# Performance work log

Hardware: AMD Instinct MI355X
Metric: run time of the kernel (lower is better)

The kernel has to match this reference:

```python
import jax, jax.numpy as jnp
import numpy as np
import math

H, D = 8, 16
O = H * D  # out_channels = 128
N_TYPES = 2
EDGE_META = [(0, 1), (1, 0)]  # (src_type, dst_type) per edge type: user->item, item->user

def _segment_softmax(alpha, dst, n):
    # PyG softmax over incoming edges grouped by destination node
    amax = jax.ops.segment_max(alpha, dst, num_segments=n)
    amax = jnp.where(jnp.isfinite(amax), amax, 0.0)
    ex = jnp.exp(alpha - amax[dst])
    den = jax.ops.segment_sum(ex, dst, num_segments=n)
    return ex / (den[dst] + 1e-16)

def setup_inputs():
    key = jax.random.key(0)
    ks = jax.random.split(key, 8)
    N, E, I = 50000, 500000, 128
    s = 1.0 / math.sqrt(I)
    sd = 1.0 / math.sqrt(D)
    return {
        "x": jax.random.normal(ks[0], (N_TYPES, N, I), jnp.float32),
        "k_w": jax.random.normal(ks[1], (N_TYPES, O, I), jnp.float32) * s,
        "k_b": jnp.zeros((N_TYPES, O), jnp.float32),
        "q_w": jax.random.normal(ks[2], (N_TYPES, O, I), jnp.float32) * s,
        "q_b": jnp.zeros((N_TYPES, O), jnp.float32),
        "v_w": jax.random.normal(ks[3], (N_TYPES, O, I), jnp.float32) * s,
        "v_b": jnp.zeros((N_TYPES, O), jnp.float32),
        "a_w": jax.random.normal(ks[4], (N_TYPES, O, O), jnp.float32) * s,
        "a_b": jnp.zeros((N_TYPES, O), jnp.float32),
        "skip": jnp.ones((N_TYPES,), jnp.float32),
        "a_rel": jax.random.normal(ks[5], (2, H, D, D), jnp.float32) * sd,
        "m_rel": jax.random.normal(ks[6], (2, H, D, D), jnp.float32) * sd,
        "p_rel": jnp.ones((2, H), jnp.float32),
        "ln_g": jnp.ones((O,), jnp.float32),
        "ln_b": jnp.zeros((O,), jnp.float32),
        "edge_index": jax.random.randint(ks[7], (2, 2, E), 0, N, jnp.int32),
    }

def reference(x, k_w, k_b, q_w, q_b, v_w, v_b, a_w, a_b, skip, a_rel, m_rel, p_rel, ln_g, ln_b, edge_index):
    N = x.shape[1]
    lin = lambda xi, w, b: xi @ w.T + b
    # per-node-type K/Q/V projections -> [T, N, H, D]
    k = jnp.stack([lin(x[t], k_w[t], k_b[t]) for t in range(N_TYPES)]).reshape(N_TYPES, N, H, D)
    q = jnp.stack([lin(x[t], q_w[t], q_b[t]) for t in range(N_TYPES)]).reshape(N_TYPES, N, H, D)
    v = jnp.stack([lin(x[t], v_w[t], v_b[t]) for t in range(N_TYPES)]).reshape(N_TYPES, N, H, D)
    agg = jnp.zeros((N_TYPES, N, O), x.dtype)
    for e, (st, dt) in enumerate(EDGE_META):
        src, dst = edge_index[e, 0], edge_index[e, 1]
        ke = jnp.einsum('nhd,hde->nhe', k[st], a_rel[e])  # relation-transformed keys
        ve = jnp.einsum('nhd,hde->nhe', v[st], m_rel[e])  # relation-transformed values
        alpha = jnp.einsum('ehd,ehd->eh', q[dt][dst], ke[src]) * p_rel[e] / math.sqrt(D)
        alpha = _segment_softmax(alpha, dst, N)  # [E, H]
        msg = (ve[src] * alpha[..., None]).reshape(-1, O)
        agg = agg.at[dt].add(jax.ops.segment_sum(msg, dst, num_segments=N))
    outs = []
    for t in range(N_TYPES):
        o = lin(jax.nn.gelu(agg[t], approximate=False), a_w[t], a_b[t])
        beta = jax.nn.sigmoid(skip[t])
        o = beta * o + (1.0 - beta) * x[t]  # HGT skip (out_channels == in_channels)
        o = jax.nn.relu(o)
        mu = jnp.mean(o, axis=-1, keepdims=True)
        var = jnp.mean((o - mu) ** 2, axis=-1, keepdims=True)
        o = (o - mu) / jnp.sqrt(var + 1e-5) * ln_g + ln_b  # LayerNorm; dropout = identity (eval)
        outs.append(o)
    return jnp.stack(outs)  # [2, N, 128]
```

## Files before the change

kernel.cpp:

```cpp
#include <hip/hip_runtime.h>
#include <math.h>


#define EB_STRIDE 40

typedef __attribute__((ext_vector_type(8))) short short8;
typedef __attribute__((ext_vector_type(4))) float floatx4;

union S8U { uint4 u; short8 s; };

__device__ __forceinline__ float bf2f(unsigned int bits16) {
  union { unsigned int i; float f; } u; u.i = bits16 << 16; return u.f;
}
__device__ __forceinline__ float bf2f_hi(unsigned int u) {
  union { unsigned int i; float f; } v; v.i = u & 0xffff0000u; return v.f;
}
__device__ __forceinline__ unsigned int f2bf(float f) {
  union { float ff; unsigned int i; } u; u.ff = f;
  unsigned int x = u.i;
  x += 0x7fffu + ((x >> 16) & 1u);
  return x >> 16;
}

__global__ void fuse_weights(
    const float* __restrict__ k_w, const float* __restrict__ k_b,
    const float* __restrict__ q_w, const float* __restrict__ q_b,
    const float* __restrict__ v_w, const float* __restrict__ v_b,
    const float* __restrict__ a_w, const float* __restrict__ a_b,
    const float* __restrict__ a_rel, const float* __restrict__ m_rel,
    const float* __restrict__ p_rel,
    unsigned short* __restrict__ Wfb, float* __restrict__ Bf,
    int* __restrict__ cnt, int nC)
{
  int tid = blockIdx.x * 256 + threadIdx.x;
  if (tid < nC) cnt[tid] = 0;
  if (tid >= 2 * 4 * 128 * 128) return;
  int t   = tid >> 16;
  int rem = tid & 65535;
  int m   = rem >> 14;
  int o   = (rem >> 7) & 127;
  int i   = rem & 127;
  float w, bias;
  if (m == 0) {
    w    = q_w[t * 16384 + o * 128 + i];
    bias = q_b[t * 128 + o];
  } else if (m == 3) {
    w    = a_w[t * 16384 + o * 128 + i];
    bias = a_b[t * 128 + o];
  } else {
    const float* bw  = (m == 1) ? k_w : v_w;
    const float* bb  = (m == 1) ? k_b : v_b;
    const float* rel = (m == 1) ? a_rel : m_rel;
    int h = o >> 4, eo = o & 15;
    float s = 0.f, sb = 0.f;
    #pragma unroll
    for (int d = 0; d < 16; ++d) {
      float r = rel[t * 2048 + h * 256 + d * 16 + eo];
      s  += bw[t * 16384 + (h * 16 + d) * 128 + i] * r;
      sb += bb[t * 128 + h * 16 + d] * r;
    }
    if (m == 1) {
      float sc = p_rel[t * 8 + h] * 0.25f;
      s *= sc; sb *= sc;
    }
    w = s; bias = sb;
  }
  Wfb[tid] = (unsigned short)f2bf(w);
  if (i == 0) Bf[t * 512 + m * 128 + o] = bias;
}

__global__ __launch_bounds__(256) void qkv_fill(
    const float* __restrict__ x, const unsigned short* __restrict__ Wfb,
    const float* __restrict__ Bf, unsigned short* __restrict__ qbuf,
    unsigned short* __restrict__ kvbuf,
    const int* __restrict__ ei, int* __restrict__ cnt, int* __restrict__ ebuf,
    int Nn, int E, int Gg)
{
  const int b = blockIdx.x;
  const int tid = threadIdx.x;

  if (b >= Gg) {
    int f = b - Gg;
    int e = f & 1;
    int i = (f >> 1) * 256 + tid;
    if (i < E) {
      int src = ei[(size_t)e * 2 * E + i];
      int dst = ei[(size_t)e * 2 * E + E + i];
      int bk = (1 - e) * Nn + dst;
      int pos = atomicAdd(&cnt[bk], 1);
      if (pos < EB_STRIDE) ebuf[(size_t)bk * EB_STRIDE + pos] = src;
    }
    return;
  }

  const int t = b & 1;
  const int m0 = (b >> 1) * 64;
  const int lane = tid & 63, w = tid >> 6;
  const int col = lane & 15, quad = lane >> 4;

  int rA = m0 + w * 16 + col;
  if (rA >= Nn) rA = Nn - 1;
  const float* arow = x + ((size_t)t * Nn + rA) * 128;

  const unsigned short* Wq = Wfb + (((size_t)(t * 4 + 0)) << 14);
  const unsigned short* Wk = Wfb + (((size_t)(t * 4 + 1)) << 14);
  const unsigned short* Wv = Wfb + (((size_t)(t * 4 + 2)) << 14);

  floatx4 aq[8], ak[8], av[8];
  #pragma unroll
  for (int ni = 0; ni < 8; ++ni) {
    aq[ni] = (floatx4)(0.f); ak[ni] = (floatx4)(0.f); av[ni] = (floatx4)(0.f);
  }

  #pragma unroll
  for (int k0 = 0; k0 < 128; k0 += 32) {
    int ko = k0 + quad * 8;
    float4 f0 = *(const float4*)(arow + ko);
    float4 f1 = *(const float4*)(arow + ko + 4);
    S8U a;
    a.u.x = f2bf(f0.x) | (f2bf(f0.y) << 16);
    a.u.y = f2bf(f0.z) | (f2bf(f0.w) << 16);
    a.u.z = f2bf(f1.x) | (f2bf(f1.y) << 16);
    a.u.w = f2bf(f1.z) | (f2bf(f1.w) << 16);
    #pragma unroll
    for (int ni = 0; ni < 8; ++ni) {
      size_t boff = (size_t)(ni * 16 + col) * 128 + ko;
      short8 bq = *(const short8*)(Wq + boff);
      short8 bk = *(const short8*)(Wk + boff);
      short8 bv = *(const short8*)(Wv + boff);
      aq[ni] = __builtin_amdgcn_mfma_f32_16x16x32_bf16(a.s, bq, aq[ni], 0, 0, 0);
      ak[ni] = __builtin_amdgcn_mfma_f32_16x16x32_bf16(a.s, bk, ak[ni], 0, 0, 0);
      av[ni] = __builtin_amdgcn_mfma_f32_16x16x32_bf16(a.s, bv, av[ni], 0, 0, 0);
    }
  }

  float bq_n[8], bk_n[8], bv_n[8];
  #pragma unroll
  for (int ni = 0; ni < 8; ++ni) {
    bq_n[ni] = Bf[t * 512 + 0 * 128 + ni * 16 + col];
    bk_n[ni] = Bf[t * 512 + 1 * 128 + ni * 16 + col];
    bv_n[ni] = Bf[t * 512 + 2 * 128 + ni * 16 + col];
  }

  unsigned int* kvp = (unsigned int*)kvbuf + ((size_t)t * Nn) * 128;
  #pragma unroll
  for (int reg = 0; reg < 4; ++reg) {
    int row = m0 + w * 16 + quad * 4 + reg;
    if (row >= Nn) continue;
    unsigned short* qp = qbuf + ((size_t)t * Nn + row) * 128 + col;
    unsigned int* cp = kvp + (size_t)row * 128 + col;
    #pragma unroll
    for (int ni = 0; ni < 8; ++ni) {
      qp[ni * 16] = (unsigned short)f2bf(aq[ni][reg] + bq_n[ni]);
      unsigned int kbits = f2bf(ak[ni][reg] + bk_n[ni]);
      unsigned int vbits = f2bf(av[ni][reg] + bv_n[ni]);
      cp[ni * 16] = (vbits << 16) | kbits;
    }
  }
}

__global__ __launch_bounds__(256) void gather_fused(
    const unsigned short* __restrict__ qbuf, const unsigned short* __restrict__ kvbuf,
    const int* __restrict__ cnt, const int* __restrict__ ebuf,
    unsigned short* __restrict__ gbuf, int N)
{
  int wid = (blockIdx.x * 256 + threadIdx.x) >> 6;
  int l = threadIdx.x & 63;
  if (wid >= 2 * N) return;
  int dt = (wid >= N) ? 1 : 0;
  int e  = 1 - dt;
  int deg = cnt[wid]; if (deg > EB_STRIDE) deg = EB_STRIDE;
  int g = l >> 4, gl = l & 15;

  uint4 qr = *(const uint4*)(qbuf + (size_t)wid * 128 + 8 * gl);
  float qv[8];
  qv[0] = bf2f(qr.x & 0xffffu); qv[1] = bf2f(qr.x >> 16);
  qv[2] = bf2f(qr.y & 0xffffu); qv[3] = bf2f(qr.y >> 16);
  qv[4] = bf2f(qr.z & 0xffffu); qv[5] = bf2f(qr.z >> 16);
  qv[6] = bf2f(qr.w & 0xffffu); qv[7] = bf2f(qr.w >> 16);

  const unsigned short* kvbase = kvbuf + ((size_t)e * N) * 256;
  const int* eb = ebuf + (size_t)wid * EB_STRIDE;
  int mysrc = (l < deg) ? eb[l] : 0;

  float acc[8];
  #pragma unroll
  for (int c = 0; c < 8; ++c) acc[c] = 0.f;
  float den = 0.f;

  for (int j0 = 0; j0 < deg; j0 += 4) {
    int j = j0 + g;
    bool valid = j < deg;
    int src = __shfl(mysrc, valid ? j : 0, 64);
    const unsigned short* kv = kvbase + (size_t)src * 256 + 16 * gl;
    uint4 a = *(const uint4*)kv;
    uint4 b = *(const uint4*)(kv + 8);
    float p;
    p = qv[0] * bf2f(a.x & 0xffffu);
    p = fmaf(qv[1], bf2f(a.y & 0xffffu), p);
    p = fmaf(qv[2], bf2f(a.z & 0xffffu), p);
    p = fmaf(qv[3], bf2f(a.w & 0xffffu), p);
    p = fmaf(qv[4], bf2f(b.x & 0xffffu), p);
    p = fmaf(qv[5], bf2f(b.y & 0xffffu), p);
    p = fmaf(qv[6], bf2f(b.z & 0xffffu), p);
    p = fmaf(qv[7], bf2f(b.w & 0xffffu), p);
    float pt = p + __shfl_xor(p, 1, 64);
    float ex = valid ? __expf(pt) : 0.f;
    den += ex;
    acc[0] = fmaf(ex, bf2f_hi(a.x), acc[0]);
    acc[1] = fmaf(ex, bf2f_hi(a.y), acc[1]);
    acc[2] = fmaf(ex, bf2f_hi(a.z), acc[2]);
    acc[3] = fmaf(ex, bf2f_hi(a.w), acc[3]);
    acc[4] = fmaf(ex, bf2f_hi(b.x), acc[4]);
    acc[5] = fmaf(ex, bf2f_hi(b.y), acc[5]);
    acc[6] = fmaf(ex, bf2f_hi(b.z), acc[6]);
    acc[7] = fmaf(ex, bf2f_hi(b.w), acc[7]);
  }

  #pragma unroll
  for (int off = 16; off < 64; off <<= 1) {
    #pragma unroll
    for (int c = 0; c < 8; ++c) acc[c] += __shfl_xor(acc[c], off, 64);
    den += __shfl_xor(den, off, 64);
  }

  if (g == 0) {
    float rden = 1.f / (den + 1e-16f);
    unsigned short r[8];
    #pragma unroll
    for (int c = 0; c < 8; ++c) {
      float gg = acc[c] * rden;
      r[c] = (unsigned short)f2bf(0.5f * gg * (1.f + erff(gg * 0.70710678118654752f)));
    }
    unsigned short* op = gbuf + (size_t)wid * 128 + 8 * gl;
    *(ushort4*)op       = make_ushort4(r[0], r[1], r[2], r[3]);
    *(ushort4*)(op + 4) = make_ushort4(r[4], r[5], r[6], r[7]);
  }
}

__global__ __launch_bounds__(256) void gemm_ln(
    const unsigned short* __restrict__ gbuf, const unsigned short* __restrict__ Wfb,
    const float* __restrict__ Bf, const float* __restrict__ x,
    const float* __restrict__ skip, const float* __restrict__ ln_g,
    const float* __restrict__ ln_b, float* __restrict__ outp, int Nn)
{
  const int tid = threadIdx.x;
  const int t = blockIdx.x & 1;
  const int m0 = (blockIdx.x >> 1) * 64;
  const int lane = tid & 63, w = tid >> 6;
  const int col = lane & 15, quad = lane >> 4;

  int rA = m0 + w * 16 + col;
  if (rA >= Nn) rA = Nn - 1;
  const unsigned short* arow = gbuf + ((size_t)t * Nn + rA) * 128;
  const unsigned short* Bm = Wfb + (((size_t)(t * 4 + 3)) << 14);

  floatx4 acc[8];
  #pragma unroll
  for (int ni = 0; ni < 8; ++ni) acc[ni] = (floatx4)(0.f);

  #pragma unroll
  for (int k0 = 0; k0 < 128; k0 += 32) {
    int ko = k0 + quad * 8;
    short8 a = *(const short8*)(arow + ko);
    #pragma unroll
    for (int ni = 0; ni < 8; ++ni) {
      short8 bb = *(const short8*)(Bm + (size_t)(ni * 16 + col) * 128 + ko);
      acc[ni] = __builtin_amdgcn_mfma_f32_16x16x32_bf16(a, bb, acc[ni], 0, 0, 0);
    }
  }

  const float* Bv = Bf + t * 512 + 3 * 128;
  float bias_n[8], g_n[8], b_n[8];
  #pragma unroll
  for (int ni = 0; ni < 8; ++ni) {
    bias_n[ni] = Bv[ni * 16 + col];
    g_n[ni]    = ln_g[ni * 16 + col];
    b_n[ni]    = ln_b[ni * 16 + col];
  }
  float sv = skip[t];
  float beta = 1.f / (1.f + __expf(-sv));
  const float* xt = x + (size_t)t * Nn * 128;
  float* op = outp + (size_t)t * Nn * 128;

  #pragma unroll
  for (int reg = 0; reg < 4; ++reg) {
    int row = m0 + w * 16 + quad * 4 + reg;
    if (row >= Nn) continue;
    const float* xr = xt + (size_t)row * 128;
    float vals[8], s = 0.f;
    #pragma unroll
    for (int ni = 0; ni < 8; ++ni) {
      float o = acc[ni][reg] + bias_n[ni];
      float v = fmaxf(beta * o + (1.f - beta) * xr[ni * 16 + col], 0.f);
      vals[ni] = v; s += v;
    }
    #pragma unroll
    for (int off = 1; off < 16; off <<= 1) s += __shfl_xor(s, off, 64);
    float mu = s * 0.0078125f;
    float sq = 0.f;
    #pragma unroll
    for (int ni = 0; ni < 8; ++ni) { float d = vals[ni] - mu; sq += d * d; }
    #pragma unroll
    for (int off = 1; off < 16; off <<= 1) sq += __shfl_xor(sq, off, 64);
    float rstd = rsqrtf(sq * 0.0078125f + 1e-5f);
    float* orow = op + (size_t)row * 128 + col;
    #pragma unroll
    for (int ni = 0; ni < 8; ++ni)
      orow[ni * 16] = (vals[ni] - mu) * rstd * g_n[ni] + b_n[ni];
  }
}

extern "C" void kernel_launch(void* const* d_in, const int* in_sizes, int n_in,
                              void* d_out, int out_size, void* d_ws, size_t ws_size,
                              hipStream_t stream) {
  const float* x     = (const float*)d_in[0];
  const float* k_w   = (const float*)d_in[1];
  const float* k_b   = (const float*)d_in[2];
  const float* q_w   = (const float*)d_in[3];
  const float* q_b   = (const float*)d_in[4];
  const float* v_w   = (const float*)d_in[5];
  const float* v_b   = (const float*)d_in[6];
  const float* a_w   = (const float*)d_in[7];
  const float* a_b   = (const float*)d_in[8];
  const float* skip  = (const float*)d_in[9];
  const float* a_rel = (const float*)d_in[10];
  const float* m_rel = (const float*)d_in[11];
  const float* p_rel = (const float*)d_in[12];
  const float* ln_g  = (const float*)d_in[13];
  const float* ln_b  = (const float*)d_in[14];
  const int* ei      = (const int*)d_in[15];
  float* out         = (float*)d_out;

  const int N = in_sizes[0] / 256;
  const int E = in_sizes[15] / 4;

  unsigned short* Wfb = (unsigned short*)d_ws;
  float* Bf = (float*)(Wfb + 2 * 4 * 128 * 128);
  unsigned short* qbuf = (unsigned short*)(Bf + 2 * 4 * 128);
  unsigned short* kvbuf = qbuf + (size_t)2 * N * 128;
  int* cnt  = (int*)(kvbuf + (size_t)2 * N * 256);
  int* ebuf = cnt + (size_t)2 * N;
  unsigned short* gbuf = (unsigned short*)(ebuf + (size_t)2 * N * EB_STRIDE);

  fuse_weights<<<(2 * 4 * 128 * 128 + 255) / 256, 256, 0, stream>>>(
      k_w, k_b, q_w, q_b, v_w, v_b, a_w, a_b, a_rel, m_rel, p_rel, Wfb, Bf,
      cnt, 2 * N);

  int Mb = (N + 63) / 64;
  int Gg = Mb * 2;
  int Fb = 2 * ((E + 255) / 256);
  qkv_fill<<<Gg + Fb, 256, 0, stream>>>(
      x, Wfb, Bf, qbuf, kvbuf, ei, cnt, ebuf, N, E, Gg);

  gather_fused<<<(2 * N * 64 + 255) / 256, 256, 0, stream>>>(
      qbuf, kvbuf, cnt, ebuf, gbuf, N);

  gemm_ln<<<Gg, 256, 0, stream>>>(
      gbuf, Wfb, Bf, x, skip, ln_g, ln_b, out, N);
}
```

Before: 350.5 us.

## Stage weight matrices in LDS and process Q/K/V projections sequentially

Result: faster. 313.9 us (-10.4%).

```diff
diff --git a/kernel.cpp b/kernel.cpp
--- a/kernel.cpp
+++ b/kernel.cpp
@@ -76,6 +76,7 @@
     const int* __restrict__ ei, int* __restrict__ cnt, int* __restrict__ ebuf,
     int Nn, int E, int Gg)
 {
+  __shared__ alignas(16) unsigned short Bls[128][136];
   const int b = blockIdx.x;
   const int tid = threadIdx.x;
 
@@ -97,24 +98,15 @@
   const int m0 = (b >> 1) * 64;
   const int lane = tid & 63, w = tid >> 6;
   const int col = lane & 15, quad = lane >> 4;
+  const int morder[3] = {1, 2, 0};
 
   int rA = m0 + w * 16 + col;
   if (rA >= Nn) rA = Nn - 1;
   const float* arow = x + ((size_t)t * Nn + rA) * 128;
-
-  const unsigned short* Wq = Wfb + (((size_t)(t * 4 + 0)) << 14);
-  const unsigned short* Wk = Wfb + (((size_t)(t * 4 + 1)) << 14);
-  const unsigned short* Wv = Wfb + (((size_t)(t * 4 + 2)) << 14);
-
-  floatx4 aq[8], ak[8], av[8];
-  #pragma unroll
-  for (int ni = 0; ni < 8; ++ni) {
-    aq[ni] = (floatx4)(0.f); ak[ni] = (floatx4)(0.f); av[ni] = (floatx4)(0.f);
-  }
-
-  #pragma unroll
-  for (int k0 = 0; k0 < 128; k0 += 32) {
-    int ko = k0 + quad * 8;
+  short8 afrag[4];
+  #pragma unroll
+  for (int kk = 0; kk < 4; ++kk) {
+    int ko = kk * 32 + quad * 8;
     float4 f0 = *(const float4*)(arow + ko);
     float4 f1 = *(const float4*)(arow + ko + 4);
     S8U a;
@@ -122,39 +114,72 @@
     a.u.y = f2bf(f0.z) | (f2bf(f0.w) << 16);
     a.u.z = f2bf(f1.x) | (f2bf(f1.y) << 16);
     a.u.w = f2bf(f1.z) | (f2bf(f1.w) << 16);
-    #pragma unroll
-    for (int ni = 0; ni < 8; ++ni) {
-      size_t boff = (size_t)(ni * 16 + col) * 128 + ko;
-      short8 bq = *(const short8*)(Wq + boff);
-      short8 bk = *(const short8*)(Wk + boff);
-      short8 bv = *(const short8*)(Wv + boff);
-      aq[ni] = __builtin_amdgcn_mfma_f32_16x16x32_bf16(a.s, bq, aq[ni], 0, 0, 0);
-      ak[ni] = __builtin_amdgcn_mfma_f32_16x16x32_bf16(a.s, bk, ak[ni], 0, 0, 0);
-      av[ni] = __builtin_amdgcn_mfma_f32_16x16x32_bf16(a.s, bv, av[ni], 0, 0, 0);
-    }
-  }
-
-  float bq_n[8], bk_n[8], bv_n[8];
-  #pragma unroll
-  for (int ni = 0; ni < 8; ++ni) {
-    bq_n[ni] = Bf[t * 512 + 0 * 128 + ni * 16 + col];
-    bk_n[ni] = Bf[t * 512 + 1 * 128 + ni * 16 + col];
-    bv_n[ni] = Bf[t * 512 + 2 * 128 + ni * 16 + col];
-  }
-
-  unsigned int* kvp = (unsigned int*)kvbuf + ((size_t)t * Nn) * 128;
-  #pragma unroll
-  for (int reg = 0; reg < 4; ++reg) {
-    int row = m0 + w * 16 + quad * 4 + reg;
-    if (row >= Nn) continue;
-    unsigned short* qp = qbuf + ((size_t)t * Nn + row) * 128 + col;
-    unsigned int* cp = kvp + (size_t)row * 128 + col;
-    #pragma unroll
-    for (int ni = 0; ni < 8; ++ni) {
-      qp[ni * 16] = (unsigned short)f2bf(aq[ni][reg] + bq_n[ni]);
-      unsigned int kbits = f2bf(ak[ni][reg] + bk_n[ni]);
-      unsigned int vbits = f2bf(av[ni][reg] + bv_n[ni]);
-      cp[ni * 16] = (vbits << 16) | kbits;
+    afrag[kk] = a.s;
+  }
+
+  unsigned int kpack[8][2];
+  float bias_n[8];
+
+  for (int mi_ = 0; mi_ < 3; ++mi_) {
+    int m = morder[mi_];
+    __syncthreads();
+    {
+      int r = tid & 127, h = tid >> 7;
+      const unsigned short* wp = Wfb + (((size_t)(t * 4 + m)) << 14) + r * 128 + h * 64;
+      #pragma unroll
+      for (int j = 0; j < 8; ++j)
+        *(uint4*)&Bls[r][h * 64 + j * 8] = ((const uint4*)wp)[j];
+    }
+    __syncthreads();
+
+    floatx4 acc[8];
+    #pragma unroll
+    for (int ni = 0; ni < 8; ++ni) acc[ni] = (floatx4)(0.f);
+
+    #pragma unroll
+    for (int kk = 0; kk < 4; ++kk) {
+      int ko = kk * 32 + quad * 8;
+      #pragma unroll
+      for (int ni = 0; ni < 8; ++ni) {
+        short8 bb = *(const short8*)&Bls[ni * 16 + col][ko];
+        acc[ni] = __builtin_amdgcn_mfma_f32_16x16x32_bf16(afrag[kk], bb, acc[ni], 0, 0, 0);
+      }
+    }
+
+    const float* Bv = Bf + t * 512 + m * 128;
+    #pragma unroll
+    for (int ni = 0; ni < 8; ++ni) bias_n[ni] = Bv[ni * 16 + col];
+
+    if (m == 1) {
+      #pragma unroll
+      for (int ni = 0; ni < 8; ++ni) {
+        kpack[ni][0] = f2bf(acc[ni][0] + bias_n[ni]) | (f2bf(acc[ni][1] + bias_n[ni]) << 16);
+        kpack[ni][1] = f2bf(acc[ni][2] + bias_n[ni]) | (f2bf(acc[ni][3] + bias_n[ni]) << 16);
+      }
+    } else if (m == 2) {
+      unsigned int* kvp = (unsigned int*)kvbuf + ((size_t)t * Nn) * 128;
+      #pragma unroll
+      for (int reg = 0; reg < 4; ++reg) {
+        int row = m0 + w * 16 + quad * 4 + reg;
+        if (row >= Nn) continue;
+        unsigned int* cp = kvp + (size_t)row * 128 + col;
+        #pragma unroll
+        for (int ni = 0; ni < 8; ++ni) {
+          unsigned int kbits = (kpack[ni][reg >> 1] >> ((reg & 1) * 16)) & 0xffffu;
+          unsigned int vbits = f2bf(acc[ni][reg] + bias_n[ni]);
+          cp[ni * 16] = (vbits << 16) | kbits;
+        }
+      }
+    } else {
+      #pragma unroll
+      for (int reg = 0; reg < 4; ++reg) {
+        int row = m0 + w * 16 + quad * 4 + reg;
+        if (row >= Nn) continue;
+        unsigned short* cp = qbuf + ((size_t)t * Nn + row) * 128 + col;
+        #pragma unroll
+        for (int ni = 0; ni < 8; ++ni)
+          cp[ni * 16] = (unsigned short)f2bf(acc[ni][reg] + bias_n[ni]);
+      }
     }
   }
 }
@@ -244,6 +269,7 @@
     const float* __restrict__ skip, const float* __restrict__ ln_g,
     const float* __restrict__ ln_b, float* __restrict__ outp, int Nn)
 {
+  __shared__ alignas(16) unsigned short Bls[128][136];
   const int tid = threadIdx.x;
   const int t = blockIdx.x & 1;
   const int m0 = (blockIdx.x >> 1) * 64;
@@ -253,20 +279,31 @@
   int rA = m0 + w * 16 + col;
   if (rA >= Nn) rA = Nn - 1;
   const unsigned short* arow = gbuf + ((size_t)t * Nn + rA) * 128;
-  const unsigned short* Bm = Wfb + (((size_t)(t * 4 + 3)) << 14);
+  short8 afrag[4];
+  #pragma unroll
+  for (int kk = 0; kk < 4; ++kk)
+    afrag[kk] = *(const short8*)(arow + kk * 32 + quad * 8);
+
+  {
+    int r = tid & 127, h = tid >> 7;
+    const unsigned short* wp = Wfb + (((size_t)(t * 4 + 3)) << 14) + r * 128 + h * 64;
+    #pragma unroll
+    for (int j = 0; j < 8; ++j)
+      *(uint4*)&Bls[r][h * 64 + j * 8] = ((const uint4*)wp)[j];
+  }
+  __syncthreads();
 
   floatx4 acc[8];
   #pragma unroll
   for (int ni = 0; ni < 8; ++ni) acc[ni] = (floatx4)(0.f);
 
   #pragma unroll
-  for (int k0 = 0; k0 < 128; k0 += 32) {
-    int ko = k0 + quad * 8;
-    short8 a = *(const short8*)(arow + ko);
+  for (int kk = 0; kk < 4; ++kk) {
+    int ko = kk * 32 + quad * 8;
     #pragma unroll
     for (int ni = 0; ni < 8; ++ni) {
-      short8 bb = *(const short8*)(Bm + (size_t)(ni * 16 + col) * 128 + ko);
-      acc[ni] = __builtin_amdgcn_mfma_f32_16x16x32_bf16(a, bb, acc[ni], 0, 0, 0);
+      short8 bb = *(const short8*)&Bls[ni * 16 + col][ko];
+      acc[ni] = __builtin_amdgcn_mfma_f32_16x16x32_bf16(afrag[kk], bb, acc[ni], 0, 0, 0);
     }
   }
 
```
